# Kernel optimization log

Measured on AMD Instinct MI355X. Metric: run time of the kernel, lower is better.

Reference implementation:

```python
import jax, jax.numpy as jnp
import numpy as np

TOPK = 2
NORM_TOPK = True
SCALE = 1.0
EPS = 1e-9


def setup_inputs() -> dict:
    key = jax.random.key(0)
    ks = jax.random.split(key, 9)
    h, i, E = 2048, 1024, 16
    std = 0.02
    return {
        "x": jax.random.normal(ks[0], (1, 2048, h), jnp.float32),
        "Wr": jax.random.normal(ks[1], (E, h), jnp.float32) * std,
        "bias": jnp.zeros((E,), jnp.float32),
        "Wg": jax.random.normal(ks[2], (E, h, i), jnp.float32) * std,
        "Wu": jax.random.normal(ks[3], (E, h, i), jnp.float32) * std,
        "Wd": jax.random.normal(ks[4], (E, i, h), jnp.float32) * std,
        "sWg": jax.random.normal(ks[5], (h, i), jnp.float32) * std,
        "sWu": jax.random.normal(ks[6], (h, i), jnp.float32) * std,
        "sWd": jax.random.normal(ks[7], (i, h), jnp.float32) * std,
    }


def reference(x, Wr, bias, Wg, Wu, Wd, sWg, sWu, sWd):
    b, s, h = x.shape
    E = Wr.shape[0]
    xt = x.reshape(b * s, h)  # [T, h]

    # Router: softmax over expert logits, then top-k
    logits = xt @ Wr.T + bias  # [T, E]
    probs = jax.nn.softmax(logits, axis=-1)
    topk_val, topk_idx = jax.lax.top_k(probs, TOPK)  # [T, K]
    if NORM_TOPK:
        w = topk_val / (jnp.sum(topk_val, axis=-1, keepdims=True) + EPS)
    else:
        w = topk_val
    w = w * SCALE

    # Dense per-expert SwiGLU (mathematically identical to gather/scatter dispatch)
    g = jnp.einsum('th,ehi->tei', xt, Wg)  # [T, E, i]
    u = jnp.einsum('th,ehi->tei', xt, Wu)
    y = jnp.einsum('tei,eih->teh', jax.nn.silu(g) * u, Wd)  # [T, E, h]

    # Combine: out[t] = sum_k w[t,k] * y[t, idx[t,k]]
    oh = jax.nn.one_hot(topk_idx, E, dtype=x.dtype)  # [T, K, E]
    routed = jnp.einsum('tke,tk,teh->th', oh, w, y)

    # Shared expert (SwiGLU)
    shared = (jax.nn.silu(xt @ sWg) * (xt @ sWu)) @ sWd

    return (routed + shared).reshape(b, s, h)
```

## Files before the change

### kernel.cpp

```cpp
#include <hip/hip_runtime.h>
#include <hip/hip_bf16.h>

#define T_TOK 2048
#define HDIM  2048
#define IDIM  1024
#define NE    16
#define NEX   17
#define NASSIGN (T_TOK*3)
#define TM    64

#define G1_NCT 16
#define G2_NCT 32
#define G1_NWG (TM*G1_NCT)
#define G2_NWG (TM*G2_NCT)

typedef __attribute__((ext_vector_type(8))) short bf16x8;
typedef __attribute__((ext_vector_type(4))) float f32x4;

#define WAITVM(N) asm volatile("s_waitcnt vmcnt(" #N ")" ::: "memory")
#define WAITLGKM  asm volatile("s_waitcnt lgkmcnt(0)" ::: "memory")
#define SCHEDB    __builtin_amdgcn_sched_barrier(0)
#define BARRIER   __builtin_amdgcn_s_barrier()

__device__ __forceinline__ unsigned short f2bf(float f) {
    union { float f; unsigned u; } v; v.f = f;
    unsigned r = v.u + 0x7fffu + ((v.u >> 16) & 1u);
    return (unsigned short)(r >> 16);
}
__device__ __forceinline__ unsigned pack2f(float a, float b) {
    __hip_bfloat162 h = __float22bfloat162_rn(float2{a, b});
    unsigned r;
    __builtin_memcpy(&r, &h, 4);
    return r;
}
__device__ __forceinline__ float fidx(const float4& v, int j) {
    return ((const float*)&v)[j];
}
__device__ __forceinline__ int SW(int r) { return (r ^ (r >> 2)) & 7; }
__device__ __forceinline__ int lds_off(int row, int kelem) {
    return (row << 7) + ((((kelem >> 3) ^ SW(row))) << 4) + ((kelem & 7) << 1);
}
__device__ __forceinline__ f32x4 mfma16(bf16x8 a, bf16x8 b, f32x4 c) {
    return __builtin_amdgcn_mfma_f32_16x16x32_bf16(a, b, c, 0, 0, 0);
}
__device__ __forceinline__ void gload_lds16(const void* g, void* lds) {
    __builtin_amdgcn_global_load_lds(
        (const __attribute__((address_space(1))) unsigned*)g,
        (__attribute__((address_space(3))) unsigned*)lds, 16, 0, 0);
}

__global__ __launch_bounds__(256) void k_cvt(const float* __restrict__ x,
                                             unsigned short* __restrict__ xbf) {
    int i = blockIdx.x * 256 + threadIdx.x;
    float4 v = ((const float4*)x)[i];
    uint2 p{pack2f(v.x, v.y), pack2f(v.z, v.w)};
    ((uint2*)xbf)[i] = p;
}

__global__ void k_router(const float* __restrict__ x, const float* __restrict__ Wr,
                         const float* __restrict__ bias, float* __restrict__ wtok,
                         int* __restrict__ idxtok, int* __restrict__ counts) {
    int t = blockIdx.x;
    int lane = threadIdx.x & 63;
    int wave = threadIdx.x >> 6;
    __shared__ float lg[NE];
    const float4* xr = (const float4*)(x + (size_t)t * HDIM);
    for (int e = wave; e < NE; e += 4) {
        const float4* wr = (const float4*)(Wr + (size_t)e * HDIM);
        float s = 0.f;
        for (int j = lane; j < HDIM / 4; j += 64) {
            float4 a = xr[j], b = wr[j];
            s += a.x*b.x + a.y*b.y + a.z*b.z + a.w*b.w;
        }
        #pragma unroll
        for (int d = 32; d; d >>= 1) s += __shfl_xor(s, d);
        if (lane == 0) lg[e] = s + bias[e];
    }
    __syncthreads();
    if (threadIdx.x == 0) {
        float m = lg[0];
        #pragma unroll
        for (int e = 1; e < NE; e++) m = fmaxf(m, lg[e]);
        float p[NE]; float S = 0.f;
        #pragma unroll
        for (int e = 0; e < NE; e++) { p[e] = expf(lg[e] - m); S += p[e]; }
        int i0 = 0;
        #pragma unroll
        for (int e = 1; e < NE; e++) if (p[e] > p[i0]) i0 = e;
        int i1 = (i0 == 0) ? 1 : 0;
        for (int e = 0; e < NE; e++) if (e != i0 && p[e] > p[i1]) i1 = e;
        float v0 = p[i0] / S, v1 = p[i1] / S;
        float wsum = v0 + v1 + 1e-9f;
        wtok[t*2+0] = v0 / wsum;
        wtok[t*2+1] = v1 / wsum;
        idxtok[t*2+0] = i0;
        idxtok[t*2+1] = i1;
        atomicAdd(&counts[i0], 1);
        atomicAdd(&counts[i1], 1);
    }
}

__global__ void k_scan(const int* __restrict__ counts, int* __restrict__ offs,
                       int* __restrict__ cursor, int4* __restrict__ tiles) {
    if (threadIdx.x == 0) {
        int acc = 0;
        for (int e = 0; e < NEX; e++) {
            offs[e] = acc; cursor[e] = acc;
            acc += (e < NE) ? counts[e] : T_TOK;
        }
        offs[NEX] = acc;
        int nt = 0;
        for (int e = 0; e < NEX; e++) {
            for (int r = offs[e]; r < offs[e+1]; r += 128) {
                tiles[nt] = int4{r, min(128, offs[e+1] - r), e, 0};
                nt++;
            }
        }
        for (; nt < TM; nt++) tiles[nt] = int4{0, 0, 0, 0};
    }
}

__global__ void k_scatter(const int* __restrict__ idxtok, const float* __restrict__ wtok,
                          int* __restrict__ cursor, const int* __restrict__ offs,
                          int* __restrict__ rows, float* __restrict__ wrow) {
    int t = blockIdx.x * blockDim.x + threadIdx.x;
    if (t >= T_TOK) return;
    #pragma unroll
    for (int k = 0; k < 2; k++) {
        int e = idxtok[t*2+k];
        int pos = atomicAdd(&cursor[e], 1);
        rows[pos] = t;
        wrow[pos] = wtok[t*2+k];
    }
    int p16 = offs[NE] + t;
    rows[p16] = t;
    wrow[p16] = 1.0f;
}

__global__ __launch_bounds__(512) void k_gemm1(
        const unsigned short* __restrict__ xbf,
        const float* __restrict__ Wg, const float* __restrict__ Wu,
        const float* __restrict__ sWg, const float* __restrict__ sWu,
        const int4* __restrict__ tiles, const int* __restrict__ rows,
        const float* __restrict__ wrow, unsigned short* __restrict__ act) {
    int bid = blockIdx.x;
    int wg = (bid & 7) * (G1_NWG >> 3) + (bid >> 3);
    int ti = wg & (TM - 1);
    int ct = wg >> 6;

    int4 tl = tiles[ti];
    int nrows = tl.y;
    if (nrows == 0) return;
    int rs = tl.x, e = tl.z;
    const float* wgp = (e < NE) ? Wg + (size_t)e * HDIM * IDIM : sWg;
    const float* wup = (e < NE) ? Wu + (size_t)e * HDIM * IDIM : sWu;
    int n0 = ct * 64;

    __shared__ unsigned short As[2][128 * 64];
    __shared__ unsigned short Bs[2][64 * 64];
    __shared__ unsigned short Us[2][64 * 64];
    __shared__ int rloc[128];

    int tid = threadIdx.x;
    if (tid < 128) rloc[tid] = rows[rs + min(tid, nrows - 1)];
    __syncthreads();

    int l = tid & 63, w = tid >> 6;
    int ar0 = w * 8 + (l >> 3);
    int ar1 = 64 + ar0;
    const unsigned short* asrc0 = xbf + (size_t)rloc[ar0] * HDIM + (((l & 7) ^ SW(ar0)) << 3);
    const unsigned short* asrc1 = xbf + (size_t)rloc[ar1] * HDIM + (((l & 7) ^ SW(ar1)) << 3);

    int n4 = (tid & 15) << 2;
    int kb = (tid >> 4) << 1;
    const float* gsrc = wgp + (size_t)kb * IDIM + n0 + n4;
    const float* usrc = wup + (size_t)kb * IDIM + n0 + n4;

    int wr = (w >> 2) << 6;
    int wc = (w & 3) << 4;
    int fr = l & 15;
    int fk = (l >> 4) << 3;

    float4 gR0, gR1, uR0, uR1;

    #define G1_LOADW(K0) do { \
        gR0 = *(const float4*)(gsrc + (size_t)(K0) * IDIM); \
        gR1 = *(const float4*)(gsrc + (size_t)(K0) * IDIM + IDIM); \
        uR0 = *(const float4*)(usrc + (size_t)(K0) * IDIM); \
        uR1 = *(const float4*)(usrc + (size_t)(K0) * IDIM + IDIM); \
    } while (0)

    #define G1_GLOADA(K0, B) do { \
        gload_lds16(asrc0 + (K0), (char*)As[B] + w * 1024); \
        gload_lds16(asrc1 + (K0), (char*)As[B] + 8192 + w * 1024); \
    } while (0)

    #define G1_WRITEW(B) do { \
        _Pragma("unroll") \
        for (int i = 0; i < 4; ++i) { \
            int n = n4 + i; \
            *(unsigned*)((char*)Bs[B] + lds_off(n, kb)) = pack2f(fidx(gR0,i), fidx(gR1,i)); \
            *(unsigned*)((char*)Us[B] + lds_off(n, kb)) = pack2f(fidx(uR0,i), fidx(uR1,i)); \
        } \
    } while (0)

    f32x4 accg[4] = {}, accu[4] = {};
    const int NK = HDIM / 64;
    const int KLAST = (NK - 1) * 64;

    G1_LOADW(0);
    G1_GLOADA(0, 0);
    SCHEDB;
    WAITVM(2);
    G1_WRITEW(0);
    G1_LOADW(64);
    SCHEDB;
    WAITVM(4);
    WAITLGKM;
    BARRIER;

    for (int k = 0; k < NK; ++k) {
        int buf = k & 1;
        int kA = min((k + 1) * 64, KLAST);
        int kW = min((k + 2) * 64, KLAST);
        G1_GLOADA(kA, buf ^ 1);
        SCHEDB;
        WAITVM(2);
        G1_WRITEW(buf ^ 1);
        G1_LOADW(kW);
        SCHEDB;
        #pragma unroll
        for (int kh = 0; kh < 2; ++kh) {
            int kk = (kh << 5) + fk;
            bf16x8 a[4], bg, bu;
            #pragma unroll
            for (int m = 0; m < 4; ++m)
                a[m] = *(const bf16x8*)((const char*)As[buf] + lds_off(wr + m * 16 + fr, kk));
            bg = *(const bf16x8*)((const char*)Bs[buf] + lds_off(wc + fr, kk));
            bu = *(const bf16x8*)((const char*)Us[buf] + lds_off(wc + fr, kk));
            #pragma unroll
            for (int m = 0; m < 4; ++m) {
                accg[m] = mfma16(a[m], bg, accg[m]);
                accu[m] = mfma16(a[m], bu, accu[m]);
            }
        }
        WAITVM(4);
        WAITLGKM;
        BARRIER;
    }
    WAITVM(0);

    int crow = (l >> 4) << 2;
    int ccol = l & 15;
    #pragma unroll
    for (int m = 0; m < 4; ++m) {
        #pragma unroll
        for (int reg = 0; reg < 4; ++reg) {
            int r = wr + m * 16 + crow + reg;
            if (r < nrows) {
                float wv = wrow[rs + r];
                float g = accg[m][reg], u = accu[m][reg];
                act[(size_t)(rs + r) * IDIM + n0 + wc + ccol] =
                    f2bf(g / (1.f + __expf(-g)) * u * wv);
            }
        }
    }
    #undef G1_LOADW
    #undef G1_GLOADA
    #undef G1_WRITEW
}

__global__ __launch_bounds__(512) void k_gemm2(
        const unsigned short* __restrict__ act,
        const float* __restrict__ Wd, const float* __restrict__ sWd,
        const int4* __restrict__ tiles, const int* __restrict__ rows,
        float* __restrict__ out) {
    int bid = blockIdx.x;
    int wg = (bid & 7) * (G2_NWG >> 3) + (bid >> 3);
    int ti = wg & (TM - 1);
    int ct = wg >> 6;

    int4 tl = tiles[ti];
    int nrows = tl.y;
    if (nrows == 0) return;
    int rs = tl.x, e = tl.z;
    const float* wdp = (e < NE) ? Wd + (size_t)e * IDIM * HDIM : sWd;
    int n0 = ct * 64;

    __shared__ unsigned short As[2][128 * 64];
    __shared__ unsigned short Bs[2][64 * 64];
    __shared__ int rloc[128];

    int tid = threadIdx.x;
    if (tid < 128) rloc[tid] = rows[rs + min(tid, nrows - 1)];
    __syncthreads();

    int l = tid & 63, w = tid >> 6;
    int ar0 = w * 8 + (l >> 3);
    int ar1 = 64 + ar0;
    const unsigned short* asrc0 = act + (size_t)(rs + ar0) * IDIM + (((l & 7) ^ SW(ar0)) << 3);
    const unsigned short* asrc1 = act + (size_t)(rs + ar1) * IDIM + (((l & 7) ^ SW(ar1)) << 3);

    int n4 = (tid & 15) << 2;
    int kb = (tid >> 4) << 1;
    const float* dsrc = wdp + (size_t)kb * HDIM + n0 + n4;

    int wr = (w >> 2) << 6;
    int wc = (w & 3) << 4;
    int fr = l & 15;
    int fk = (l >> 4) << 3;

    float4 dR0, dR1;

    #define G2_LOADW(K0) do { \
        dR0 = *(const float4*)(dsrc + (size_t)(K0) * HDIM); \
        dR1 = *(const float4*)(dsrc + (size_t)(K0) * HDIM + HDIM); \
    } while (0)

    #define G2_GLOADA(K0, B) do { \
        gload_lds16(asrc0 + (K0), (char*)As[B] + w * 1024); \
        gload_lds16(asrc1 + (K0), (char*)As[B] + 8192 + w * 1024); \
    } while (0)

    #define G2_WRITEW(B) do { \
        _Pragma("unroll") \
        for (int i = 0; i < 4; ++i) { \
            int n = n4 + i; \
            *(unsigned*)((char*)Bs[B] + lds_off(n, kb)) = pack2f(fidx(dR0,i), fidx(dR1,i)); \
        } \
    } while (0)

    f32x4 acc[4] = {};
    const int NK = IDIM / 64;
    const int KLAST = (NK - 1) * 64;

    G2_LOADW(0);
    G2_GLOADA(0, 0);
    SCHEDB;
    WAITVM(2);
    G2_WRITEW(0);
    G2_LOADW(64);
    SCHEDB;
    WAITVM(2);
    WAITLGKM;
    BARRIER;

    for (int k = 0; k < NK; ++k) {
        int buf = k & 1;
        int kA = min((k + 1) * 64, KLAST);
        int kW = min((k + 2) * 64, KLAST);
        G2_GLOADA(kA, buf ^ 1);
        SCHEDB;
        WAITVM(2);
        G2_WRITEW(buf ^ 1);
        G2_LOADW(kW);
        SCHEDB;
        #pragma unroll
        for (int kh = 0; kh < 2; ++kh) {
            int kk = (kh << 5) + fk;
            bf16x8 a[4], b;
            #pragma unroll
            for (int m = 0; m < 4; ++m)
                a[m] = *(const bf16x8*)((const char*)As[buf] + lds_off(wr + m * 16 + fr, kk));
            b = *(const bf16x8*)((const char*)Bs[buf] + lds_off(wc + fr, kk));
            #pragma unroll
            for (int m = 0; m < 4; ++m)
                acc[m] = mfma16(a[m], b, acc[m]);
        }
        WAITVM(2);
        WAITLGKM;
        BARRIER;
    }
    WAITVM(0);

    int crow = (l >> 4) << 2;
    int ccol = l & 15;
    #pragma unroll
    for (int m = 0; m < 4; ++m) {
        #pragma unroll
        for (int reg = 0; reg < 4; ++reg) {
            int r = wr + m * 16 + crow + reg;
            if (r < nrows) {
                atomicAdd(&out[(size_t)rloc[r] * HDIM + n0 + wc + ccol], acc[m][reg]);
            }
        }
    }
    #undef G2_LOADW
    #undef G2_GLOADA
    #undef G2_WRITEW
}

extern "C" void kernel_launch(void* const* d_in, const int* in_sizes, int n_in,
                              void* d_out, int out_size, void* d_ws, size_t ws_size,
                              hipStream_t stream) {
    const float* x    = (const float*)d_in[0];
    const float* Wr   = (const float*)d_in[1];
    const float* bias = (const float*)d_in[2];
    const float* Wg   = (const float*)d_in[3];
    const float* Wu   = (const float*)d_in[4];
    const float* Wd   = (const float*)d_in[5];
    const float* sWg  = (const float*)d_in[6];
    const float* sWu  = (const float*)d_in[7];
    const float* sWd  = (const float*)d_in[8];
    float* out = (float*)d_out;

    char* p = (char*)d_ws;
    int*   counts = (int*)p;                 p += 256;
    int*   offs   = (int*)p;                 p += 256;
    int*   cursor = (int*)p;                 p += 256;
    int4*  tiles  = (int4*)p;                p += TM * sizeof(int4);
    int*   idxtok = (int*)p;                 p += (size_t)T_TOK * 2 * sizeof(int);
    float* wtok   = (float*)p;               p += (size_t)T_TOK * 2 * sizeof(float);
    int*   rows   = (int*)p;                 p += (size_t)NASSIGN * sizeof(int);
    float* wrow   = (float*)p;               p += (size_t)NASSIGN * sizeof(float);
    unsigned short* act = (unsigned short*)p; p += (size_t)NASSIGN * IDIM * sizeof(unsigned short);
    unsigned short* xbf = (unsigned short*)p;

    hipMemsetAsync(counts, 0, 256, stream);
    hipMemsetAsync(d_out, 0, (size_t)out_size * sizeof(float), stream);

    k_cvt<<<dim3(T_TOK * HDIM / 1024), dim3(256), 0, stream>>>(x, xbf);
    k_router<<<dim3(T_TOK), dim3(256), 0, stream>>>(x, Wr, bias, wtok, idxtok, counts);
    k_scan<<<dim3(1), dim3(64), 0, stream>>>(counts, offs, cursor, tiles);
    k_scatter<<<dim3((T_TOK + 255) / 256), dim3(256), 0, stream>>>(idxtok, wtok, cursor, offs, rows, wrow);
    k_gemm1<<<dim3(G1_NWG), dim3(512), 0, stream>>>(xbf, Wg, Wu, sWg, sWu, tiles, rows, wrow, act);
    k_gemm2<<<dim3(G2_NWG), dim3(512), 0, stream>>>(act, Wd, sWd, tiles, rows, out);
}
```

Baseline: 325.4 us.

## Deepen weight-register prefetch to two stages in both MoE GEMM kernels

Both grouped GEMM kernels now keep two register stages for the fp32 weight tiles, loading weights three k-steps ahead instead of two. The main loop is unrolled by two so the register stage and LDS buffer indices are compile-time constants. The wait before writing weights to LDS is dropped from inside each step, giving global loads more time to land before conversion. This adds weight registers per thread, which can reduce occupancy or cause spills at 512 threads, and the reworked vmcnt accounting must stay correct.

New measurement: 334.1 us. +2.7%, slower.

```diff
diff --git a/kernel.cpp b/kernel.cpp
--- a/kernel.cpp
+++ b/kernel.cpp
@@ -181,13 +181,13 @@
     int fr = l & 15;
     int fk = (l >> 4) << 3;
 
-    float4 gR0, gR1, uR0, uR1;
-
-    #define G1_LOADW(K0) do { \
-        gR0 = *(const float4*)(gsrc + (size_t)(K0) * IDIM); \
-        gR1 = *(const float4*)(gsrc + (size_t)(K0) * IDIM + IDIM); \
-        uR0 = *(const float4*)(usrc + (size_t)(K0) * IDIM); \
-        uR1 = *(const float4*)(usrc + (size_t)(K0) * IDIM + IDIM); \
+    float4 gR[2][2], uR[2][2];
+
+    #define G1_LOADW(K0, S) do { \
+        gR[S][0] = *(const float4*)(gsrc + (size_t)(K0) * IDIM); \
+        gR[S][1] = *(const float4*)(gsrc + (size_t)(K0) * IDIM + IDIM); \
+        uR[S][0] = *(const float4*)(usrc + (size_t)(K0) * IDIM); \
+        uR[S][1] = *(const float4*)(usrc + (size_t)(K0) * IDIM + IDIM); \
     } while (0)
 
     #define G1_GLOADA(K0, B) do { \
@@ -195,58 +195,64 @@
         gload_lds16(asrc1 + (K0), (char*)As[B] + 8192 + w * 1024); \
     } while (0)
 
-    #define G1_WRITEW(B) do { \
+    #define G1_WRITEW(S, B) do { \
         _Pragma("unroll") \
         for (int i = 0; i < 4; ++i) { \
             int n = n4 + i; \
-            *(unsigned*)((char*)Bs[B] + lds_off(n, kb)) = pack2f(fidx(gR0,i), fidx(gR1,i)); \
-            *(unsigned*)((char*)Us[B] + lds_off(n, kb)) = pack2f(fidx(uR0,i), fidx(uR1,i)); \
+            *(unsigned*)((char*)Bs[B] + lds_off(n, kb)) = pack2f(fidx(gR[S][0],i), fidx(gR[S][1],i)); \
+            *(unsigned*)((char*)Us[B] + lds_off(n, kb)) = pack2f(fidx(uR[S][0],i), fidx(uR[S][1],i)); \
         } \
+    } while (0)
+
+    #define G1_MFMA(B) do { \
+        _Pragma("unroll") \
+        for (int kh = 0; kh < 2; ++kh) { \
+            int kk = (kh << 5) + fk; \
+            bf16x8 a[4], bg, bu; \
+            _Pragma("unroll") \
+            for (int m = 0; m < 4; ++m) \
+                a[m] = *(const bf16x8*)((const char*)As[B] + lds_off(wr + m * 16 + fr, kk)); \
+            bg = *(const bf16x8*)((const char*)Bs[B] + lds_off(wc + fr, kk)); \
+            bu = *(const bf16x8*)((const char*)Us[B] + lds_off(wc + fr, kk)); \
+            _Pragma("unroll") \
+            for (int m = 0; m < 4; ++m) { \
+                accg[m] = mfma16(a[m], bg, accg[m]); \
+                accu[m] = mfma16(a[m], bu, accu[m]); \
+            } \
+        } \
+    } while (0)
+
+    #define G1_STEP(K, S, BC, BN) do { \
+        G1_GLOADA(min(((K)+1)*64, KLAST), BN); \
+        G1_WRITEW(S, BN); \
+        G1_LOADW(min(((K)+3)*64, KLAST), S); \
+        SCHEDB; \
+        G1_MFMA(BC); \
+        SCHEDB; \
+        WAITVM(4); \
+        WAITLGKM; \
+        BARRIER; \
     } while (0)
 
     f32x4 accg[4] = {}, accu[4] = {};
     const int NK = HDIM / 64;
     const int KLAST = (NK - 1) * 64;
 
-    G1_LOADW(0);
+    G1_LOADW(0, 0);
+    G1_LOADW(64, 1);
     G1_GLOADA(0, 0);
     SCHEDB;
-    WAITVM(2);
-    G1_WRITEW(0);
-    G1_LOADW(64);
+    WAITVM(6);
+    G1_WRITEW(0, 0);
+    G1_LOADW(128, 0);
     SCHEDB;
     WAITVM(4);
     WAITLGKM;
     BARRIER;
 
-    for (int k = 0; k < NK; ++k) {
-        int buf = k & 1;
-        int kA = min((k + 1) * 64, KLAST);
-        int kW = min((k + 2) * 64, KLAST);
-        G1_GLOADA(kA, buf ^ 1);
-        SCHEDB;
-        WAITVM(2);
-        G1_WRITEW(buf ^ 1);
-        G1_LOADW(kW);
-        SCHEDB;
-        #pragma unroll
-        for (int kh = 0; kh < 2; ++kh) {
-            int kk = (kh << 5) + fk;
-            bf16x8 a[4], bg, bu;
-            #pragma unroll
-            for (int m = 0; m < 4; ++m)
-                a[m] = *(const bf16x8*)((const char*)As[buf] + lds_off(wr + m * 16 + fr, kk));
-            bg = *(const bf16x8*)((const char*)Bs[buf] + lds_off(wc + fr, kk));
-            bu = *(const bf16x8*)((const char*)Us[buf] + lds_off(wc + fr, kk));
-            #pragma unroll
-            for (int m = 0; m < 4; ++m) {
-                accg[m] = mfma16(a[m], bg, accg[m]);
-                accu[m] = mfma16(a[m], bu, accu[m]);
-            }
-        }
-        WAITVM(4);
-        WAITLGKM;
-        BARRIER;
+    for (int k = 0; k < NK; k += 2) {
+        G1_STEP(k,     1, 0, 1);
+        G1_STEP(k + 1, 0, 1, 0);
     }
     WAITVM(0);
 
@@ -268,6 +274,8 @@
     #undef G1_LOADW
     #undef G1_GLOADA
     #undef G1_WRITEW
+    #undef G1_MFMA
+    #undef G1_STEP
 }
 
 __global__ __launch_bounds__(512) void k_gemm2(
@@ -310,11 +318,11 @@
     int fr = l & 15;
     int fk = (l >> 4) << 3;
 
-    float4 dR0, dR1;
-
-    #define G2_LOADW(K0) do { \
-        dR0 = *(const float4*)(dsrc + (size_t)(K0) * HDIM); \
-        dR1 = *(const float4*)(dsrc + (size_t)(K0) * HDIM + HDIM); \
+    float4 dR[2][2];
+
+    #define G2_LOADW(K0, S) do { \
+        dR[S][0] = *(const float4*)(dsrc + (size_t)(K0) * HDIM); \
+        dR[S][1] = *(const float4*)(dsrc + (size_t)(K0) * HDIM + HDIM); \
     } while (0)
 
     #define G2_GLOADA(K0, B) do { \
@@ -322,54 +330,60 @@
         gload_lds16(asrc1 + (K0), (char*)As[B] + 8192 + w * 1024); \
     } while (0)
 
-    #define G2_WRITEW(B) do { \
+    #define G2_WRITEW(S, B) do { \
         _Pragma("unroll") \
         for (int i = 0; i < 4; ++i) { \
             int n = n4 + i; \
-            *(unsigned*)((char*)Bs[B] + lds_off(n, kb)) = pack2f(fidx(dR0,i), fidx(dR1,i)); \
+            *(unsigned*)((char*)Bs[B] + lds_off(n, kb)) = pack2f(fidx(dR[S][0],i), fidx(dR[S][1],i)); \
         } \
+    } while (0)
+
+    #define G2_MFMA(B) do { \
+        _Pragma("unroll") \
+        for (int kh = 0; kh < 2; ++kh) { \
+            int kk = (kh << 5) + fk; \
+            bf16x8 a[4], b; \
+            _Pragma("unroll") \
+            for (int m = 0; m < 4; ++m) \
+                a[m] = *(const bf16x8*)((const char*)As[B] + lds_off(wr + m * 16 + fr, kk)); \
+            b = *(const bf16x8*)((const char*)Bs[B] + lds_off(wc + fr, kk)); \
+            _Pragma("unroll") \
+            for (int m = 0; m < 4; ++m) \
+                acc[m] = mfma16(a[m], b, acc[m]); \
+        } \
+    } while (0)
+
+    #define G2_STEP(K, S, BC, BN) do { \
+        G2_GLOADA(min(((K)+1)*64, KLAST), BN); \
+        G2_WRITEW(S, BN); \
+        G2_LOADW(min(((K)+3)*64, KLAST), S); \
+        SCHEDB; \
+        G2_MFMA(BC); \
+        SCHEDB; \
+        WAITVM(2); \
+        WAITLGKM; \
+        BARRIER; \
     } while (0)
 
     f32x4 acc[4] = {};
     const int NK = IDIM / 64;
     const int KLAST = (NK - 1) * 64;
 
-    G2_LOADW(0);
+    G2_LOADW(0, 0);
+    G2_LOADW(64, 1);
     G2_GLOADA(0, 0);
     SCHEDB;
-    WAITVM(2);
-    G2_WRITEW(0);
-    G2_LOADW(64);
+    WAITVM(4);
+    G2_WRITEW(0, 0);
+    G2_LOADW(128, 0);
     SCHEDB;
     WAITVM(2);
     WAITLGKM;
     BARRIER;
 
-    for (int k = 0; k < NK; ++k) {
-        int buf = k & 1;
-        int kA = min((k + 1) * 64, KLAST);
-        int kW = min((k + 2) * 64, KLAST);
-        G2_GLOADA(kA, buf ^ 1);
-        SCHEDB;
-        WAITVM(2);
-        G2_WRITEW(buf ^ 1);
-        G2_LOADW(kW);
-        SCHEDB;
-        #pragma unroll
-        for (int kh = 0; kh < 2; ++kh) {
-            int kk = (kh << 5) + fk;
-            bf16x8 a[4], b;
-            #pragma unroll
-            for (int m = 0; m < 4; ++m)
-                a[m] = *(const bf16x8*)((const char*)As[buf] + lds_off(wr + m * 16 + fr, kk));
-            b = *(const bf16x8*)((const char*)Bs[buf] + lds_off(wc + fr, kk));
-            #pragma unroll
-            for (int m = 0; m < 4; ++m)
-                acc[m] = mfma16(a[m], b, acc[m]);
-        }
-        WAITVM(2);
-        WAITLGKM;
-        BARRIER;
+    for (int k = 0; k < NK; k += 2) {
+        G2_STEP(k,     1, 0, 1);
+        G2_STEP(k + 1, 0, 1, 0);
     }
     WAITVM(0);
 
@@ -388,6 +402,8 @@
     #undef G2_LOADW
     #undef G2_GLOADA
     #undef G2_WRITEW
+    #undef G2_MFMA
+    #undef G2_STEP
 }
 
 extern "C" void kernel_launch(void* const* d_in, const int* in_sizes, int n_in,
```

## Load A fragments directly from global and halve K step in MoE GEMMs

Applied to the files above, without the earlier changes.

Both grouped GEMMs drop the LDS staging of the activation (A) tile. Each wave now loads its bf16 A fragments straight from global memory into registers, with double buffering in registers. The K step shrinks from 64 to 32, and the weight tile moves to a padded 80-byte-stride LDS layout in place of the XOR swizzle. The wave layout changes to 32x32 per wave with a 2x2 MFMA grid, cutting LDS footprint and LDS read traffic for A. In exchange, waves sharing the same rows re-read A from global/L1, and the smaller K step doubles the number of barriers.

Result: slower. 439.2 us, median of 3 (+35.0%).

```diff
diff --git a/kernel.cpp b/kernel.cpp
--- a/kernel.cpp
+++ b/kernel.cpp
@@ -9,16 +9,14 @@
 #define NASSIGN (T_TOK*3)
 #define TM    64
 
-#define G1_NCT 16
-#define G2_NCT 32
-#define G1_NWG (TM*G1_NCT)
-#define G2_NWG (TM*G2_NCT)
+#define G1_NWG (TM*16)
+#define G2_NWG (TM*32)
 
 typedef __attribute__((ext_vector_type(8))) short bf16x8;
 typedef __attribute__((ext_vector_type(4))) float f32x4;
 
-#define WAITVM(N) asm volatile("s_waitcnt vmcnt(" #N ")" ::: "memory")
-#define WAITLGKM  asm volatile("s_waitcnt lgkmcnt(0)" ::: "memory")
+#define WAITVM0   asm volatile("s_waitcnt vmcnt(0)" ::: "memory")
+#define WAITLGKM0 asm volatile("s_waitcnt lgkmcnt(0)" ::: "memory")
 #define SCHEDB    __builtin_amdgcn_sched_barrier(0)
 #define BARRIER   __builtin_amdgcn_s_barrier()
 
@@ -33,20 +31,8 @@
     __builtin_memcpy(&r, &h, 4);
     return r;
 }
-__device__ __forceinline__ float fidx(const float4& v, int j) {
-    return ((const float*)&v)[j];
-}
-__device__ __forceinline__ int SW(int r) { return (r ^ (r >> 2)) & 7; }
-__device__ __forceinline__ int lds_off(int row, int kelem) {
-    return (row << 7) + ((((kelem >> 3) ^ SW(row))) << 4) + ((kelem & 7) << 1);
-}
 __device__ __forceinline__ f32x4 mfma16(bf16x8 a, bf16x8 b, f32x4 c) {
     return __builtin_amdgcn_mfma_f32_16x16x32_bf16(a, b, c, 0, 0, 0);
-}
-__device__ __forceinline__ void gload_lds16(const void* g, void* lds) {
-    __builtin_amdgcn_global_load_lds(
-        (const __attribute__((address_space(1))) unsigned*)g,
-        (__attribute__((address_space(3))) unsigned*)lds, 16, 0, 0);
 }
 
 __global__ __launch_bounds__(256) void k_cvt(const float* __restrict__ x,
@@ -156,9 +142,8 @@
     const float* wup = (e < NE) ? Wu + (size_t)e * HDIM * IDIM : sWu;
     int n0 = ct * 64;
 
-    __shared__ unsigned short As[2][128 * 64];
-    __shared__ unsigned short Bs[2][64 * 64];
-    __shared__ unsigned short Us[2][64 * 64];
+    __shared__ unsigned short Bs[2][64 * 40];
+    __shared__ unsigned short Us[2][64 * 40];
     __shared__ int rloc[128];
 
     int tid = threadIdx.x;
@@ -166,108 +151,120 @@
     __syncthreads();
 
     int l = tid & 63, w = tid >> 6;
-    int ar0 = w * 8 + (l >> 3);
-    int ar1 = 64 + ar0;
-    const unsigned short* asrc0 = xbf + (size_t)rloc[ar0] * HDIM + (((l & 7) ^ SW(ar0)) << 3);
-    const unsigned short* asrc1 = xbf + (size_t)rloc[ar1] * HDIM + (((l & 7) ^ SW(ar1)) << 3);
-
-    int n4 = (tid & 15) << 2;
-    int kb = (tid >> 4) << 1;
-    const float* gsrc = wgp + (size_t)kb * IDIM + n0 + n4;
-    const float* usrc = wup + (size_t)kb * IDIM + n0 + n4;
-
-    int wr = (w >> 2) << 6;
-    int wc = (w & 3) << 4;
+    int wr = (w >> 1) << 5;
+    int wc = (w & 1) << 5;
     int fr = l & 15;
     int fk = (l >> 4) << 3;
 
-    float4 gR0, gR1, uR0, uR1;
-
-    #define G1_LOADW(K0) do { \
-        gR0 = *(const float4*)(gsrc + (size_t)(K0) * IDIM); \
-        gR1 = *(const float4*)(gsrc + (size_t)(K0) * IDIM + IDIM); \
-        uR0 = *(const float4*)(usrc + (size_t)(K0) * IDIM); \
-        uR1 = *(const float4*)(usrc + (size_t)(K0) * IDIM + IDIM); \
-    } while (0)
-
-    #define G1_GLOADA(K0, B) do { \
-        gload_lds16(asrc0 + (K0), (char*)As[B] + w * 1024); \
-        gload_lds16(asrc1 + (K0), (char*)As[B] + 8192 + w * 1024); \
-    } while (0)
-
+    const unsigned short* ap0 = xbf + (size_t)rloc[wr + fr] * HDIM + fk;
+    const unsigned short* ap1 = xbf + (size_t)rloc[wr + 16 + fr] * HDIM + fk;
+
+    int n2 = (tid & 31) << 1;
+    int kb = (tid >> 5) << 1;
+    const float* gsrc = wgp + (size_t)kb * IDIM + n0 + n2;
+    const float* usrc = wup + (size_t)kb * IDIM + n0 + n2;
+    int wb0 = n2 * 80 + kb * 2;
+    int wb1 = wb0 + 80;
+
+    int ro0 = (wc + fr) * 80 + fk * 2;
+    int ro1 = (wc + 16 + fr) * 80 + fk * 2;
+
+    float2 g0, g1, u0, u1;
+    bf16x8 aP0, aP1, aQ0, aQ1;
+    f32x4 accg[2][2] = {}, accu[2][2] = {};
+
+    const int NK = HDIM / 32;
+    const int KL = (NK - 1) * 32;
+
+    #define G1_LOADW(KE) do { \
+        g0 = *(const float2*)(gsrc + (size_t)(KE) * IDIM); \
+        g1 = *(const float2*)(gsrc + (size_t)(KE) * IDIM + IDIM); \
+        u0 = *(const float2*)(usrc + (size_t)(KE) * IDIM); \
+        u1 = *(const float2*)(usrc + (size_t)(KE) * IDIM + IDIM); \
+    } while (0)
     #define G1_WRITEW(B) do { \
-        _Pragma("unroll") \
-        for (int i = 0; i < 4; ++i) { \
-            int n = n4 + i; \
-            *(unsigned*)((char*)Bs[B] + lds_off(n, kb)) = pack2f(fidx(gR0,i), fidx(gR1,i)); \
-            *(unsigned*)((char*)Us[B] + lds_off(n, kb)) = pack2f(fidx(uR0,i), fidx(uR1,i)); \
-        } \
-    } while (0)
-
-    f32x4 accg[4] = {}, accu[4] = {};
-    const int NK = HDIM / 64;
-    const int KLAST = (NK - 1) * 64;
+        *(unsigned*)((char*)Bs[B] + wb0) = pack2f(g0.x, g1.x); \
+        *(unsigned*)((char*)Bs[B] + wb1) = pack2f(g0.y, g1.y); \
+        *(unsigned*)((char*)Us[B] + wb0) = pack2f(u0.x, u1.x); \
+        *(unsigned*)((char*)Us[B] + wb1) = pack2f(u0.y, u1.y); \
+    } while (0)
+    #define G1_COMPUTE(B, A0, A1) do { \
+        bf16x8 b0 = *(const bf16x8*)((const char*)Bs[B] + ro0); \
+        bf16x8 v0 = *(const bf16x8*)((const char*)Us[B] + ro0); \
+        accg[0][0] = mfma16(A0, b0, accg[0][0]); \
+        accg[1][0] = mfma16(A1, b0, accg[1][0]); \
+        accu[0][0] = mfma16(A0, v0, accu[0][0]); \
+        accu[1][0] = mfma16(A1, v0, accu[1][0]); \
+        bf16x8 b1 = *(const bf16x8*)((const char*)Bs[B] + ro1); \
+        bf16x8 v1 = *(const bf16x8*)((const char*)Us[B] + ro1); \
+        accg[0][1] = mfma16(A0, b1, accg[0][1]); \
+        accg[1][1] = mfma16(A1, b1, accg[1][1]); \
+        accu[0][1] = mfma16(A0, v1, accu[0][1]); \
+        accu[1][1] = mfma16(A1, v1, accu[1][1]); \
+    } while (0)
 
     G1_LOADW(0);
-    G1_GLOADA(0, 0);
+    G1_WRITEW(0);
+    aP0 = *(const bf16x8*)(ap0);
+    aP1 = *(const bf16x8*)(ap1);
+    G1_LOADW(32);
+    WAITLGKM0;
+    BARRIER;
     SCHEDB;
-    WAITVM(2);
-    G1_WRITEW(0);
-    G1_LOADW(64);
-    SCHEDB;
-    WAITVM(4);
-    WAITLGKM;
-    BARRIER;
-
-    for (int k = 0; k < NK; ++k) {
-        int buf = k & 1;
-        int kA = min((k + 1) * 64, KLAST);
-        int kW = min((k + 2) * 64, KLAST);
-        G1_GLOADA(kA, buf ^ 1);
-        SCHEDB;
-        WAITVM(2);
-        G1_WRITEW(buf ^ 1);
-        G1_LOADW(kW);
-        SCHEDB;
-        #pragma unroll
-        for (int kh = 0; kh < 2; ++kh) {
-            int kk = (kh << 5) + fk;
-            bf16x8 a[4], bg, bu;
-            #pragma unroll
-            for (int m = 0; m < 4; ++m)
-                a[m] = *(const bf16x8*)((const char*)As[buf] + lds_off(wr + m * 16 + fr, kk));
-            bg = *(const bf16x8*)((const char*)Bs[buf] + lds_off(wc + fr, kk));
-            bu = *(const bf16x8*)((const char*)Us[buf] + lds_off(wc + fr, kk));
-            #pragma unroll
-            for (int m = 0; m < 4; ++m) {
-                accg[m] = mfma16(a[m], bg, accg[m]);
-                accu[m] = mfma16(a[m], bu, accu[m]);
-            }
-        }
-        WAITVM(4);
-        WAITLGKM;
-        BARRIER;
-    }
-    WAITVM(0);
+
+    for (int k = 0; k < NK; k += 2) {
+        {
+            int kA = min(k + 1, NK - 1) * 32;
+            int kW = min(k + 2, NK - 1) * 32;
+            G1_WRITEW(1);
+            aQ0 = *(const bf16x8*)(ap0 + kA);
+            aQ1 = *(const bf16x8*)(ap1 + kA);
+            G1_LOADW(kW);
+            SCHEDB;
+            G1_COMPUTE(0, aP0, aP1);
+            SCHEDB;
+            WAITLGKM0;
+            BARRIER;
+            SCHEDB;
+        }
+        {
+            int kA = min(k + 2, NK - 1) * 32;
+            int kW = min(k + 3, NK - 1) * 32;
+            G1_WRITEW(0);
+            aP0 = *(const bf16x8*)(ap0 + kA);
+            aP1 = *(const bf16x8*)(ap1 + kA);
+            G1_LOADW(kW);
+            SCHEDB;
+            G1_COMPUTE(1, aQ0, aQ1);
+            SCHEDB;
+            WAITLGKM0;
+            BARRIER;
+            SCHEDB;
+        }
+    }
+    WAITVM0;
 
     int crow = (l >> 4) << 2;
     int ccol = l & 15;
     #pragma unroll
-    for (int m = 0; m < 4; ++m) {
+    for (int m = 0; m < 2; ++m) {
         #pragma unroll
         for (int reg = 0; reg < 4; ++reg) {
             int r = wr + m * 16 + crow + reg;
             if (r < nrows) {
                 float wv = wrow[rs + r];
-                float g = accg[m][reg], u = accu[m][reg];
-                act[(size_t)(rs + r) * IDIM + n0 + wc + ccol] =
-                    f2bf(g / (1.f + __expf(-g)) * u * wv);
+                #pragma unroll
+                for (int n = 0; n < 2; ++n) {
+                    float g = accg[m][n][reg], u = accu[m][n][reg];
+                    act[(size_t)(rs + r) * IDIM + n0 + wc + n * 16 + ccol] =
+                        f2bf(g / (1.f + __expf(-g)) * u * wv);
+                }
             }
         }
     }
     #undef G1_LOADW
-    #undef G1_GLOADA
     #undef G1_WRITEW
+    #undef G1_COMPUTE
 }
 
 __global__ __launch_bounds__(512) void k_gemm2(
@@ -287,107 +284,108 @@
     const float* wdp = (e < NE) ? Wd + (size_t)e * IDIM * HDIM : sWd;
     int n0 = ct * 64;
 
-    __shared__ unsigned short As[2][128 * 64];
-    __shared__ unsigned short Bs[2][64 * 64];
-    __shared__ int rloc[128];
+    __shared__ unsigned short Bs[2][64 * 40];
 
     int tid = threadIdx.x;
-    if (tid < 128) rloc[tid] = rows[rs + min(tid, nrows - 1)];
-    __syncthreads();
-
     int l = tid & 63, w = tid >> 6;
-    int ar0 = w * 8 + (l >> 3);
-    int ar1 = 64 + ar0;
-    const unsigned short* asrc0 = act + (size_t)(rs + ar0) * IDIM + (((l & 7) ^ SW(ar0)) << 3);
-    const unsigned short* asrc1 = act + (size_t)(rs + ar1) * IDIM + (((l & 7) ^ SW(ar1)) << 3);
-
-    int n4 = (tid & 15) << 2;
-    int kb = (tid >> 4) << 1;
-    const float* dsrc = wdp + (size_t)kb * HDIM + n0 + n4;
-
-    int wr = (w >> 2) << 6;
-    int wc = (w & 3) << 4;
+    int wr = (w >> 1) << 5;
+    int wc = (w & 1) << 5;
     int fr = l & 15;
     int fk = (l >> 4) << 3;
 
-    float4 dR0, dR1;
-
-    #define G2_LOADW(K0) do { \
-        dR0 = *(const float4*)(dsrc + (size_t)(K0) * HDIM); \
-        dR1 = *(const float4*)(dsrc + (size_t)(K0) * HDIM + HDIM); \
-    } while (0)
-
-    #define G2_GLOADA(K0, B) do { \
-        gload_lds16(asrc0 + (K0), (char*)As[B] + w * 1024); \
-        gload_lds16(asrc1 + (K0), (char*)As[B] + 8192 + w * 1024); \
-    } while (0)
-
+    const unsigned short* ap0 = act + (size_t)(rs + min(wr + fr, nrows - 1)) * IDIM + fk;
+    const unsigned short* ap1 = act + (size_t)(rs + min(wr + 16 + fr, nrows - 1)) * IDIM + fk;
+
+    int n2 = (tid & 31) << 1;
+    int kb = (tid >> 5) << 1;
+    const float* dsrc = wdp + (size_t)kb * HDIM + n0 + n2;
+    int wb0 = n2 * 80 + kb * 2;
+    int wb1 = wb0 + 80;
+
+    int ro0 = (wc + fr) * 80 + fk * 2;
+    int ro1 = (wc + 16 + fr) * 80 + fk * 2;
+
+    float2 d0, d1;
+    bf16x8 aP0, aP1, aQ0, aQ1;
+    f32x4 acc[2][2] = {};
+
+    const int NK = IDIM / 32;
+
+    #define G2_LOADW(KE) do { \
+        d0 = *(const float2*)(dsrc + (size_t)(KE) * HDIM); \
+        d1 = *(const float2*)(dsrc + (size_t)(KE) * HDIM + HDIM); \
+    } while (0)
     #define G2_WRITEW(B) do { \
-        _Pragma("unroll") \
-        for (int i = 0; i < 4; ++i) { \
-            int n = n4 + i; \
-            *(unsigned*)((char*)Bs[B] + lds_off(n, kb)) = pack2f(fidx(dR0,i), fidx(dR1,i)); \
-        } \
-    } while (0)
-
-    f32x4 acc[4] = {};
-    const int NK = IDIM / 64;
-    const int KLAST = (NK - 1) * 64;
+        *(unsigned*)((char*)Bs[B] + wb0) = pack2f(d0.x, d1.x); \
+        *(unsigned*)((char*)Bs[B] + wb1) = pack2f(d0.y, d1.y); \
+    } while (0)
+    #define G2_COMPUTE(B, A0, A1) do { \
+        bf16x8 b0 = *(const bf16x8*)((const char*)Bs[B] + ro0); \
+        acc[0][0] = mfma16(A0, b0, acc[0][0]); \
+        acc[1][0] = mfma16(A1, b0, acc[1][0]); \
+        bf16x8 b1 = *(const bf16x8*)((const char*)Bs[B] + ro1); \
+        acc[0][1] = mfma16(A0, b1, acc[0][1]); \
+        acc[1][1] = mfma16(A1, b1, acc[1][1]); \
+    } while (0)
 
     G2_LOADW(0);
-    G2_GLOADA(0, 0);
+    G2_WRITEW(0);
+    aP0 = *(const bf16x8*)(ap0);
+    aP1 = *(const bf16x8*)(ap1);
+    G2_LOADW(32);
+    WAITLGKM0;
+    BARRIER;
     SCHEDB;
-    WAITVM(2);
-    G2_WRITEW(0);
-    G2_LOADW(64);
-    SCHEDB;
-    WAITVM(2);
-    WAITLGKM;
-    BARRIER;
-
-    for (int k = 0; k < NK; ++k) {
-        int buf = k & 1;
-        int kA = min((k + 1) * 64, KLAST);
-        int kW = min((k + 2) * 64, KLAST);
-        G2_GLOADA(kA, buf ^ 1);
-        SCHEDB;
-        WAITVM(2);
-        G2_WRITEW(buf ^ 1);
-        G2_LOADW(kW);
-        SCHEDB;
-        #pragma unroll
-        for (int kh = 0; kh < 2; ++kh) {
-            int kk = (kh << 5) + fk;
-            bf16x8 a[4], b;
-            #pragma unroll
-            for (int m = 0; m < 4; ++m)
-                a[m] = *(const bf16x8*)((const char*)As[buf] + lds_off(wr + m * 16 + fr, kk));
-            b = *(const bf16x8*)((const char*)Bs[buf] + lds_off(wc + fr, kk));
-            #pragma unroll
-            for (int m = 0; m < 4; ++m)
-                acc[m] = mfma16(a[m], b, acc[m]);
-        }
-        WAITVM(2);
-        WAITLGKM;
-        BARRIER;
-    }
-    WAITVM(0);
+
+    for (int k = 0; k < NK; k += 2) {
+        {
+            int kA = min(k + 1, NK - 1) * 32;
+            int kW = min(k + 2, NK - 1) * 32;
+            G2_WRITEW(1);
+            aQ0 = *(const bf16x8*)(ap0 + kA);
+            aQ1 = *(const bf16x8*)(ap1 + kA);
+            G2_LOADW(kW);
+            SCHEDB;
+            G2_COMPUTE(0, aP0, aP1);
+            SCHEDB;
+            WAITLGKM0;
+            BARRIER;
+            SCHEDB;
+        }
+        {
+            int kA = min(k + 2, NK - 1) * 32;
+            int kW = min(k + 3, NK - 1) * 32;
+            G2_WRITEW(0);
+            aP0 = *(const bf16x8*)(ap0 + kA);
+            aP1 = *(const bf16x8*)(ap1 + kA);
+            G2_LOADW(kW);
+            SCHEDB;
+            G2_COMPUTE(1, aQ0, aQ1);
+            SCHEDB;
+            WAITLGKM0;
+            BARRIER;
+            SCHEDB;
+        }
+    }
+    WAITVM0;
 
     int crow = (l >> 4) << 2;
     int ccol = l & 15;
     #pragma unroll
-    for (int m = 0; m < 4; ++m) {
+    for (int m = 0; m < 2; ++m) {
         #pragma unroll
         for (int reg = 0; reg < 4; ++reg) {
             int r = wr + m * 16 + crow + reg;
             if (r < nrows) {
-                atomicAdd(&out[(size_t)rloc[r] * HDIM + n0 + wc + ccol], acc[m][reg]);
+                size_t base = (size_t)rows[rs + r] * HDIM + n0 + wc + ccol;
+                atomicAdd(&out[base], acc[m][0][reg]);
+                atomicAdd(&out[base + 16], acc[m][1][reg]);
             }
         }
     }
     #undef G2_LOADW
-    #undef G2_GLOADA
     #undef G2_WRITEW
+    #undef G2_COMPUTE
 }
 
 extern "C" void kernel_launch(void* const* d_in, const int* in_sizes, int n_in,
```
